# Kernel optimization log

Hardware: AMD Instinct MI355X
Metric: run time of the kernel (lower is better)

The kernel has to match this reference:

```python
import jax, jax.numpy as jnp
import numpy as np

BATCH = 16384
EPS = 1e-5


def _pool22_sum(x):
    # 4 * AvgPool2d((2,2),stride 2) == sum over 2x2 blocks. x: [B,1,h,w]
    B, C, h, w = x.shape
    return x.reshape(B, C, h // 2, 2, w // 2, 2).sum(axis=(3, 5))


def _transform(img, ans):
    # img: [B,h,h]. Faithful port of `transfrom`: zero border rows/cols, then
    # 10 quadratic features per 2x2 patch, laid out as [B,1,k,10k] with last
    # axis index = patch_col*10 + feature.
    B, h, w = img.shape
    if ans in ('top_bottom', 'all'):
        m = jnp.ones((h, 1), img.dtype).at[0].set(0).at[-1].set(0)
        img = img * m
    if ans in ('left_right', 'all'):
        m = jnp.ones((1, w), img.dtype).at[:, 0].set(0).at[:, -1].set(0)
        img = img * m
    k = h // 2
    p = img.reshape(B, k, 2, k, 2)
    b00 = p[:, :, 0, :, 0]; b01 = p[:, :, 0, :, 1]
    b10 = p[:, :, 1, :, 0]; b11 = p[:, :, 1, :, 1]
    prods = jnp.stack([
        b00 * b00, b01 * b01, b10 * b10, b11 * b11,
        b00 * b01, b00 * b10, b00 * b11,
        b01 * b10, b01 * b11, b10 * b11], axis=-1)  # [B,k,k,10]
    return prods.reshape(B, 1, k, 10 * k)


def _pool110_sum(a):
    # 10 * AvgPool2d((1,10),stride(1,10)) == sum over groups of 10 on last axis
    B, C, k, tk = a.shape
    return a.reshape(B, C, k, tk // 10, 10).sum(-1)


def _bn(x, gamma, beta):
    # BatchNorm2d(1) in training mode: batch stats over (N,H,W), biased var
    m = x.mean(axis=(0, 2, 3), keepdims=True)
    v = jnp.mean((x - m) ** 2, axis=(0, 2, 3), keepdims=True)
    g = gamma.reshape(1, -1, 1, 1)
    b = beta.reshape(1, -1, 1, 1)
    return (x - m) * jax.lax.rsqrt(v + EPS) * g + b


def setup_inputs() -> dict:
    key = jax.random.key(0)
    ks = jax.random.split(key, 16)

    def xavier(k, shape):
        fan_in, fan_out = shape[-1], shape[-2]
        std = np.sqrt(2.0 / (fan_in + fan_out))
        return jax.random.normal(k, shape, jnp.float32) * std

    return {
        'x': jax.random.normal(ks[0], (BATCH, 1, 28, 28), jnp.float32),
        'l1_w1': xavier(ks[1], (1, 28, 28)),
        'l1_w2_1': xavier(ks[2], (1, 14, 140)),
        'l1_w2_2': xavier(ks[3], (1, 14, 140)),
        'l1_w2_3': xavier(ks[4], (1, 14, 140)),
        'l1_w2_4': xavier(ks[5], (1, 14, 140)),
        'l1_w3': xavier(ks[6], (1, 14, 14)),
        'l2_w1': xavier(ks[7], (1, 14, 14)),
        'l2_w2': xavier(ks[8], (1, 7, 70)),
        'l2_w4': xavier(ks[9], (1, 7, 7)),
        'w_fc1': jax.random.normal(ks[10], (10, 49), jnp.float32) / np.sqrt(49.0),
        'b_fc1': jnp.zeros((10,), jnp.float32),
        'w_fc2': jax.random.normal(ks[11], (10, 2401), jnp.float32) / np.sqrt(2401.0),
        'b_fc2': jnp.zeros((10,), jnp.float32),
        'bn_gamma': jnp.ones((1,), jnp.float32),
        'bn_beta': jnp.zeros((1,), jnp.float32),
    }


def reference(x, l1_w1, l1_w2_1, l1_w2_2, l1_w2_3, l1_w2_4, l1_w3,
              l2_w1, l2_w2, l2_w4, w_fc1, b_fc1, w_fc2, b_fc2,
              bn_gamma, bn_beta):
    B = x.shape[0]
    img = x[:, 0]  # [B,28,28]
    # layer 1
    l1 = _pool22_sum(x * l1_w1)
    for W, ans in ((l1_w2_1, 'left_right'), (l1_w2_2, 'top_bottom'),
                   (l1_w2_3, 'all'), (l1_w2_4, 'none')):
        l1 = l1 + _pool110_sum(_transform(img, ans) * W)
    l1 = l1 + l1_w3  # [B,1,14,14]
    h = _bn(l1, bn_gamma, bn_beta)
    # layer 2
    l2 = _pool22_sum(h * l2_w1) + _pool110_sum(_transform(h[:, 0], 'none') * l2_w2) + l2_w4
    h = _bn(l2, bn_gamma, bn_beta)  # [B,1,7,7]
    # layer 3
    l3_x1 = h.reshape(B, -1) @ w_fc1.T + b_fc1
    v = h.reshape(B, 49)
    c = jnp.triu(v[:, :, None] * v[:, None, :])  # [B,49,49], trans_all_rg
    l3_x2 = c.reshape(B, -1) @ w_fc2.T + b_fc2
    return l3_x1 + l3_x2
```

## Files before the change

kernel.cpp:

```cpp
#include <hip/hip_runtime.h>

#define BATCH 16384
#define N1 (BATCH * 196)
#define N2 (BATCH * 49)
#define S1 8
#define NREC 80

#define WS_P1_OFF    0
#define WS_P2_OFF    32768
#define WS_WREC_OFF  65536
#define WS_L1G_OFF   262144
#define WS_L2G_OFF   6684672

__device__ __forceinline__ unsigned short f2bf(float f) {
    unsigned u = __float_as_uint(f);
    unsigned r = (u + 0x7FFFu + ((u >> 16) & 1u)) >> 16;
    return (unsigned short)r;
}
__device__ __forceinline__ float bf2f(unsigned short h) {
    return __uint_as_float((unsigned)h << 16);
}
__device__ __forceinline__ float rfl_f(float v) {
    return __uint_as_float(__builtin_amdgcn_readfirstlane(__float_as_uint(v)));
}

__global__ void __launch_bounds__(256) k1(
        const float* __restrict__ x,
        const float* __restrict__ l1w1, const float* __restrict__ wA,
        const float* __restrict__ wB, const float* __restrict__ wC,
        const float* __restrict__ wD, const float* __restrict__ l1w3,
        const float* __restrict__ wf2, const float* __restrict__ wfc1,
        unsigned short* __restrict__ l1g, double* __restrict__ partials1,
        float* __restrict__ wrec) {
    __shared__ __align__(16) float xs[S1 * 784];
    __shared__ float wls[4], wlss[4];
    int t = threadIdx.x;

    const float4* src = (const float4*)(x + (size_t)blockIdx.x * (S1 * 784));
    float4 rbuf[6];
    #pragma unroll
    for (int i = 0; i < 6; ++i) rbuf[i] = src[t + 256 * i];
    float4 rtail;
    if (t < 32) rtail = src[t + 1536];

    bool active = t < 196;
    int pos = active ? t : 0;
    int pi = pos / 14, pj = pos - 14 * pi;
    int r0 = (2 * pi) * 28 + 2 * pj;
    float4 a0, a1, a2, a3;
    {
        float2 wt = *(const float2*)(l1w1 + r0);
        float2 wb = *(const float2*)(l1w1 + r0 + 28);
        a0 = make_float4(wt.x, wt.y, wb.x, wb.y);
        float mA0 = (pj != 0) ? 1.f : 0.f, mA1 = (pj != 13) ? 1.f : 0.f;
        float mB0 = (pi != 0) ? 1.f : 0.f, mB1 = (pi != 13) ? 1.f : 0.f;
        float eA[4] = {mA0, mA1, mA0, mA1};
        float eB[4] = {mB0, mB0, mB1, mB1};
        const int e1i[10] = {0,1,2,3,0,0,0,1,1,2};
        const int e2i[10] = {0,1,2,3,1,2,3,2,3,3};
        int wo = pi * 140 + 10 * pj;
        float wq[10];
        #pragma unroll
        for (int k = 0; k < 10; ++k) {
            float ca = eA[e1i[k]] * eA[e2i[k]];
            float cb = eB[e1i[k]] * eB[e2i[k]];
            wq[k] = wA[wo + k] * ca + wB[wo + k] * cb
                  + wC[wo + k] * ca * cb + wD[wo + k];
        }
        a1 = make_float4(wq[0], wq[1], wq[2], wq[3]);
        a2 = make_float4(wq[4], wq[5], wq[6], wq[7]);
        a3 = make_float4(wq[8], wq[9], l1w3[pos], 0.f);
    }

    float4* dst = (float4*)xs;
    #pragma unroll
    for (int i = 0; i < 6; ++i) dst[t + 256 * i] = rbuf[i];
    if (t < 32) dst[t + 1536] = rtail;
    __syncthreads();

    float accs[S1];
    float sum = 0.f, sumsq = 0.f;
    #pragma unroll
    for (int s = 0; s < S1; ++s) {
        const float* xb = xs + s * 784;
        float2 tp = *(const float2*)(xb + r0);
        float2 bo = *(const float2*)(xb + r0 + 28);
        float b00 = tp.x, b01 = tp.y, b10 = bo.x, b11 = bo.y;
        float acc = b00 * a0.x + b01 * a0.y + b10 * a0.z + b11 * a0.w;
        acc += b00 * b00 * a1.x + b01 * b01 * a1.y + b10 * b10 * a1.z + b11 * b11 * a1.w;
        acc += b00 * b01 * a2.x + b00 * b10 * a2.y + b00 * b11 * a2.z + b01 * b10 * a2.w;
        acc += b01 * b11 * a3.x + b10 * b11 * a3.y + a3.z;
        accs[s] = acc;
        if (active) { sum += acc; sumsq += acc * acc; }
    }

    __syncthreads();
    unsigned short* ob = (unsigned short*)xs;
    if (active) {
        int g = ((pi >> 1) * 7 + (pj >> 1)) * 4 + (pi & 1) * 2 + (pj & 1);
        #pragma unroll
        for (int s = 0; s < S1; ++s) ob[s * 196 + g] = f2bf(accs[s]);
    }
    __syncthreads();
    const unsigned int* ob32 = (const unsigned int*)ob;
    unsigned int* gout = (unsigned int*)(l1g + (size_t)blockIdx.x * (S1 * 196));
    #pragma unroll
    for (int r2 = 0; r2 < 3; ++r2) gout[t + 256 * r2] = ob32[t + 256 * r2];
    if (t < 16) gout[t + 768] = ob32[t + 768];

    #pragma unroll
    for (int off = 32; off; off >>= 1) {
        sum += __shfl_down(sum, off);
        sumsq += __shfl_down(sumsq, off);
    }
    int lane = t & 63, wid = t >> 6;
    if (lane == 0) { wls[wid] = sum; wlss[wid] = sumsq; }
    __syncthreads();
    if (t == 0) {
        partials1[blockIdx.x * 2]     = (double)(wls[0] + wls[1] + wls[2] + wls[3]);
        partials1[blockIdx.x * 2 + 1] = (double)(wlss[0] + wlss[1] + wlss[2] + wlss[3]);
    }

    if (blockIdx.x < 5) {
        int e = blockIdx.x * 256 + t;
        if (e < 1280) {
            int w = e / NREC, j = e - w * NREC;
            int i = j * 16 + w;
            float wv[10];
            int ip = 0, iq = 0;
            if (i < 1225) {
                int rem = i, p = 0;
                while (rem >= 49 - p) { rem -= 49 - p; ++p; }
                int q = p + rem;
                #pragma unroll
                for (int o = 0; o < 10; ++o) wv[o] = wf2[o * 2401 + p * 49 + q];
                ip = p * 64; iq = q * 64;
            } else if (i < 1274) {
                int k = i - 1225;
                #pragma unroll
                for (int o = 0; o < 10; ++o) wv[o] = wfc1[o * 49 + k];
                ip = k * 64; iq = 49 * 64;
            } else {
                #pragma unroll
                for (int o = 0; o < 10; ++o) wv[o] = 0.f;
            }
            float* r = wrec + (size_t)e * 12;
            #pragma unroll
            for (int o = 0; o < 10; ++o) r[o] = wv[o];
            ((int*)r)[10] = ip;
            ((int*)r)[11] = iq;
        }
    }
}

__global__ void __launch_bounds__(256) k2(
        const unsigned short* __restrict__ l1g,
        const float* __restrict__ l2w1, const float* __restrict__ l2w2,
        const float* __restrict__ l2w4,
        const float* __restrict__ gamma, const float* __restrict__ beta,
        const double* __restrict__ partials1, double* __restrict__ partials2,
        float* __restrict__ l2g) {
    __shared__ float wls[4], wlss[4];
    __shared__ double dred[8];
    __shared__ float bcast[2];
    int t = threadIdx.x;
    int lane = t & 63, wid = t >> 6;
    int sbase = blockIdx.x * S1;

    bool active = t < 196;
    int tt = active ? t : 0;
    int sub = tt / 49;
    int pos = tt - 49 * sub;

    ushort4 u0 = *(const ushort4*)(l1g + ((size_t)(sbase + sub) * 49 + pos) * 4);
    ushort4 u1 = *(const ushort4*)(l1g + ((size_t)(sbase + 4 + sub) * 49 + pos) * 4);

    {
        double s = 0.0, ss = 0.0;
        const double* p1 = partials1 + t * 16;
        #pragma unroll
        for (int k = 0; k < 8; ++k) { s += p1[k * 2]; ss += p1[k * 2 + 1]; }
        #pragma unroll
        for (int off = 32; off; off >>= 1) {
            s += __shfl_down(s, off);
            ss += __shfl_down(ss, off);
        }
        if (lane == 0) { dred[wid * 2] = s; dred[wid * 2 + 1] = ss; }
        __syncthreads();
        if (t == 0) {
            double S = dred[0] + dred[2] + dred[4] + dred[6];
            double SS = dred[1] + dred[3] + dred[5] + dred[7];
            double mean = S / (double)N1;
            double var = SS / (double)N1 - mean * mean;
            float a = (float)((double)gamma[0] / sqrt(var + 1e-5));
            bcast[0] = a;
            bcast[1] = beta[0] - (float)mean * a;
        }
    }

    int pi = pos / 7, pj = pos - 7 * pi;
    int r0 = (2 * pi) * 14 + 2 * pj;
    float4 a0 = make_float4(l2w1[r0], l2w1[r0 + 1], l2w1[r0 + 14], l2w1[r0 + 15]);
    int wo = pi * 70 + 10 * pj;
    float4 q1 = make_float4(l2w2[wo],     l2w2[wo + 1], l2w2[wo + 2], l2w2[wo + 3]);
    float4 q2 = make_float4(l2w2[wo + 4], l2w2[wo + 5], l2w2[wo + 6], l2w2[wo + 7]);
    float4 q3 = make_float4(l2w2[wo + 8], l2w2[wo + 9], l2w4[pos], 0.f);
    __syncthreads();
    float a1 = bcast[0], c1 = bcast[1];

    float sum = 0.f, sumsq = 0.f;
    #pragma unroll
    for (int s2 = 0; s2 < 2; ++s2) {
        ushort4 u = s2 ? u1 : u0;
        int smp = sbase + s2 * 4 + sub;
        float h00 = fmaf(a1, bf2f(u.x), c1), h01 = fmaf(a1, bf2f(u.y), c1);
        float h10 = fmaf(a1, bf2f(u.z), c1), h11 = fmaf(a1, bf2f(u.w), c1);
        float acc = h00 * a0.x + h01 * a0.y + h10 * a0.z + h11 * a0.w;
        acc += h00 * h00 * q1.x + h01 * h01 * q1.y + h10 * h10 * q1.z + h11 * h11 * q1.w;
        acc += h00 * h01 * q2.x + h00 * h10 * q2.y + h00 * h11 * q2.z + h01 * h10 * q2.w;
        acc += h01 * h11 * q3.x + h10 * h11 * q3.y + q3.z;
        if (active) {
            l2g[(size_t)smp * 52 + pos] = acc;
            sum += acc;
            sumsq += acc * acc;
        }
    }

    #pragma unroll
    for (int off = 32; off; off >>= 1) {
        sum += __shfl_down(sum, off);
        sumsq += __shfl_down(sumsq, off);
    }
    if (lane == 0) { wls[wid] = sum; wlss[wid] = sumsq; }
    __syncthreads();
    if (t == 0) {
        partials2[blockIdx.x * 2]     = (double)(wls[0] + wls[1] + wls[2] + wls[3]);
        partials2[blockIdx.x * 2 + 1] = (double)(wlss[0] + wlss[1] + wlss[2] + wlss[3]);
    }
}

__global__ void __launch_bounds__(1024) k3(
        const float* __restrict__ l2g, const float* __restrict__ wrec,
        const float* __restrict__ b_fc1, const float* __restrict__ b_fc2,
        const float* __restrict__ gamma, const float* __restrict__ beta,
        const double* __restrict__ partials2, float* __restrict__ out) {
    __shared__ float part[16][64][10];
    __shared__ float vsm[50 * 64];
    __shared__ double dred[32];
    __shared__ float bcast[2];
    int t = threadIdx.x, lane = t & 63, wid = t >> 6;

    float4 val;
    int vs_s = 0, vs_k4 = 0;
    if (t < 832) {
        vs_s = t / 13;
        vs_k4 = t - vs_s * 13;
        val = ((const float4*)(l2g + (size_t)blockIdx.x * 64 * 52))[vs_s * 13 + vs_k4];
    }

    {
        const double* p2 = partials2 + t * 4;
        double sd = p2[0] + p2[2], ssd = p2[1] + p2[3];
        #pragma unroll
        for (int off = 32; off; off >>= 1) {
            sd += __shfl_down(sd, off);
            ssd += __shfl_down(ssd, off);
        }
        if (lane == 0) { dred[wid * 2] = sd; dred[wid * 2 + 1] = ssd; }
        __syncthreads();
        if (t == 0) {
            double S = 0.0, SS = 0.0;
            #pragma unroll
            for (int w = 0; w < 16; ++w) { S += dred[w * 2]; SS += dred[w * 2 + 1]; }
            double mean = S / (double)N2;
            double var = SS / (double)N2 - mean * mean;
            float a = (float)((double)gamma[0] / sqrt(var + 1e-5));
            bcast[0] = a;
            bcast[1] = beta[0] - (float)mean * a;
        }
        __syncthreads();
    }
    float a2 = bcast[0], c2 = bcast[1];

    if (t < 832) {
        float vv[4] = {val.x, val.y, val.z, val.w};
        #pragma unroll
        for (int j = 0; j < 4; ++j) {
            int p = vs_k4 * 4 + j;
            if (p < 49) vsm[p * 64 + vs_s] = fmaf(a2, vv[j], c2);
        }
    }
    if (t < 64) vsm[49 * 64 + t] = 1.f;
    __syncthreads();

    float acc[10];
    #pragma unroll
    for (int o = 0; o < 10; ++o) acc[o] = 0.f;

    int W = __builtin_amdgcn_readfirstlane(wid);
    const float* base = wrec + (size_t)W * NREC * 12;
    #pragma unroll 4
    for (int j = 0; j < NREC; ++j) {
        const float* rec = base + j * 12;
        int ip = __builtin_amdgcn_readfirstlane(((const int*)rec)[10]);
        int iq = __builtin_amdgcn_readfirstlane(((const int*)rec)[11]);
        float pv = vsm[ip + lane] * vsm[iq + lane];
        #pragma unroll
        for (int o = 0; o < 10; ++o) acc[o] = fmaf(pv, rfl_f(rec[o]), acc[o]);
    }

    #pragma unroll
    for (int o = 0; o < 10; ++o) part[wid][lane][o] = acc[o];
    __syncthreads();

    if (t < 640) {
        int sl = t / 10, o = t - 10 * sl;
        float r2 = 0.f;
        #pragma unroll
        for (int w = 0; w < 16; ++w) r2 += part[w][sl][o];
        out[(size_t)(blockIdx.x * 64 + sl) * 10 + o] = r2 + b_fc1[o] + b_fc2[o];
    }
}

extern "C" void kernel_launch(void* const* d_in, const int* in_sizes, int n_in,
                              void* d_out, int out_size, void* d_ws, size_t ws_size,
                              hipStream_t stream) {
    const float* x       = (const float*)d_in[0];
    const float* l1_w1   = (const float*)d_in[1];
    const float* l1_w2_1 = (const float*)d_in[2];
    const float* l1_w2_2 = (const float*)d_in[3];
    const float* l1_w2_3 = (const float*)d_in[4];
    const float* l1_w2_4 = (const float*)d_in[5];
    const float* l1_w3   = (const float*)d_in[6];
    const float* l2_w1   = (const float*)d_in[7];
    const float* l2_w2   = (const float*)d_in[8];
    const float* l2_w4   = (const float*)d_in[9];
    const float* w_fc1   = (const float*)d_in[10];
    const float* b_fc1   = (const float*)d_in[11];
    const float* w_fc2   = (const float*)d_in[12];
    const float* b_fc2   = (const float*)d_in[13];
    const float* bn_gamma = (const float*)d_in[14];
    const float* bn_beta  = (const float*)d_in[15];

    char* ws = (char*)d_ws;
    double* partials1 = (double*)(ws + WS_P1_OFF);
    double* partials2 = (double*)(ws + WS_P2_OFF);
    float* wrec = (float*)(ws + WS_WREC_OFF);
    unsigned short* l1g = (unsigned short*)(ws + WS_L1G_OFF);
    float* l2g = (float*)(ws + WS_L2G_OFF);
    float* out = (float*)d_out;

    k1<<<BATCH / S1, 256, 0, stream>>>(x, l1_w1, l1_w2_1, l1_w2_2, l1_w2_3, l1_w2_4,
                                       l1_w3, w_fc2, w_fc1, l1g, partials1, wrec);
    k2<<<BATCH / S1, 256, 0, stream>>>(l1g, l2_w1, l2_w2, l2_w4, bn_gamma, bn_beta,
                                       partials1, partials2, l2g);
    k3<<<BATCH / 64, 1024, 0, stream>>>(l2g, wrec, b_fc1, b_fc2,
                                        bn_gamma, bn_beta, partials2, out);
}
```

Measured before the change: 42.88 us.

## Fuse layer-2 into quadratic FC kernel via BN-affine algebraic decomposition

Uses the fact that the second batch norm is affine (h = a*v + c) to expand the quadratic FC layer into terms in raw v: v_p*v_q, linear v_k terms and a constant. The per-sample sums can then be computed before the global BN-2 statistics exist. This lets layer 2 be fused into the FC kernel, which removes the l2g round trip through global memory. A light epilogue kernel combines the three partial sums with the BN scalars once the stats are known. The costs are writing 30 partials per sample, extra precomputed weight tables, and possible float cancellation error from the expanded form.

Result: slower. 107.0 us (+149.6%).

```diff
diff --git a/kernel.cpp b/kernel.cpp
--- a/kernel.cpp
+++ b/kernel.cpp
@@ -4,13 +4,14 @@
 #define N1 (BATCH * 196)
 #define N2 (BATCH * 49)
 #define S1 8
-#define NREC 80
 
 #define WS_P1_OFF    0
 #define WS_P2_OFF    32768
-#define WS_WREC_OFF  65536
-#define WS_L1G_OFF   262144
-#define WS_L2G_OFF   6684672
+#define WS_WREC_OFF  40960
+#define WS_RTAB_OFF  102400
+#define WS_WFC1S_OFF 104448
+#define WS_FCP_OFF   131072
+#define WS_L1G_OFF   4194304
 
 __device__ __forceinline__ unsigned short f2bf(float f) {
     unsigned u = __float_as_uint(f);
@@ -31,7 +32,8 @@
         const float* __restrict__ wD, const float* __restrict__ l1w3,
         const float* __restrict__ wf2, const float* __restrict__ wfc1,
         unsigned short* __restrict__ l1g, double* __restrict__ partials1,
-        float* __restrict__ wrec) {
+        float* __restrict__ wrec, float* __restrict__ rtab,
+        float* __restrict__ wfc1s) {
     __shared__ __align__(16) float xs[S1 * 784];
     __shared__ float wls[4], wlss[4];
     int t = threadIdx.x;
@@ -123,144 +125,96 @@
 
     if (blockIdx.x < 5) {
         int e = blockIdx.x * 256 + t;
-        if (e < 1280) {
-            int w = e / NREC, j = e - w * NREC;
-            int i = j * 16 + w;
-            float wv[10];
-            int ip = 0, iq = 0;
-            if (i < 1225) {
-                int rem = i, p = 0;
-                while (rem >= 49 - p) { rem -= 49 - p; ++p; }
-                int q = p + rem;
-                #pragma unroll
-                for (int o = 0; o < 10; ++o) wv[o] = wf2[o * 2401 + p * 49 + q];
-                ip = p * 64; iq = q * 64;
-            } else if (i < 1274) {
-                int k = i - 1225;
-                #pragma unroll
-                for (int o = 0; o < 10; ++o) wv[o] = wfc1[o * 49 + k];
-                ip = k * 64; iq = 49 * 64;
-            } else {
-                #pragma unroll
-                for (int o = 0; o < 10; ++o) wv[o] = 0.f;
+        int w = e / 80, j = e - w * 80;
+        int i = j * 16 + w;
+        float wv[10];
+        int ip = 0, iq = 0;
+        if (j < 77 && i < 1225) {
+            int rem = i, p = 0;
+            while (rem >= 49 - p) { rem -= 49 - p; ++p; }
+            int q = p + rem;
+            #pragma unroll
+            for (int o = 0; o < 10; ++o) wv[o] = wf2[o * 2401 + p * 49 + q];
+            ip = p * 65; iq = q * 65;
+        } else {
+            #pragma unroll
+            for (int o = 0; o < 10; ++o) wv[o] = 0.f;
+        }
+        float* r = wrec + (size_t)e * 12;
+        #pragma unroll
+        for (int o = 0; o < 10; ++o) r[o] = wv[o];
+        ((int*)r)[10] = ip;
+        ((int*)r)[11] = iq;
+    } else if (blockIdx.x == 5) {
+        #pragma unroll
+        for (int rep = 0; rep < 2; ++rep) {
+            int id = rep * 256 + t;
+            if (id < 490) {
+                int k = id / 10, o = id - k * 10;
+                const float* row = wf2 + (size_t)o * 2401;
+                float r = 2.f * row[k * 49 + k];
+                for (int q = k + 1; q < 49; ++q) r += row[k * 49 + q];
+                for (int p = 0; p < k; ++p) r += row[p * 49 + k];
+                rtab[id] = r;
             }
-            float* r = wrec + (size_t)e * 12;
-            #pragma unroll
-            for (int o = 0; o < 10; ++o) r[o] = wv[o];
-            ((int*)r)[10] = ip;
-            ((int*)r)[11] = iq;
-        }
-    }
-}
-
-__global__ void __launch_bounds__(256) k2(
+        }
+    } else if (blockIdx.x == 6) {
+        #pragma unroll
+        for (int rep = 0; rep < 2; ++rep) {
+            int id = rep * 256 + t;
+            if (id < 490) {
+                int k = id / 10, o = id - k * 10;
+                wfc1s[id] = wfc1[o * 49 + k];
+            }
+        }
+    }
+}
+
+__global__ void __launch_bounds__(1024) k2(
         const unsigned short* __restrict__ l1g,
         const float* __restrict__ l2w1, const float* __restrict__ l2w2,
         const float* __restrict__ l2w4,
         const float* __restrict__ gamma, const float* __restrict__ beta,
         const double* __restrict__ partials1, double* __restrict__ partials2,
-        float* __restrict__ l2g) {
-    __shared__ float wls[4], wlss[4];
-    __shared__ double dred[8];
-    __shared__ float bcast[2];
-    int t = threadIdx.x;
-    int lane = t & 63, wid = t >> 6;
-    int sbase = blockIdx.x * S1;
-
-    bool active = t < 196;
-    int tt = active ? t : 0;
-    int sub = tt / 49;
-    int pos = tt - 49 * sub;
-
-    ushort4 u0 = *(const ushort4*)(l1g + ((size_t)(sbase + sub) * 49 + pos) * 4);
-    ushort4 u1 = *(const ushort4*)(l1g + ((size_t)(sbase + 4 + sub) * 49 + pos) * 4);
-
-    {
-        double s = 0.0, ss = 0.0;
-        const double* p1 = partials1 + t * 16;
-        #pragma unroll
-        for (int k = 0; k < 8; ++k) { s += p1[k * 2]; ss += p1[k * 2 + 1]; }
-        #pragma unroll
-        for (int off = 32; off; off >>= 1) {
-            s += __shfl_down(s, off);
-            ss += __shfl_down(ss, off);
-        }
-        if (lane == 0) { dred[wid * 2] = s; dred[wid * 2 + 1] = ss; }
-        __syncthreads();
-        if (t == 0) {
-            double S = dred[0] + dred[2] + dred[4] + dred[6];
-            double SS = dred[1] + dred[3] + dred[5] + dred[7];
-            double mean = S / (double)N1;
-            double var = SS / (double)N1 - mean * mean;
-            float a = (float)((double)gamma[0] / sqrt(var + 1e-5));
-            bcast[0] = a;
-            bcast[1] = beta[0] - (float)mean * a;
-        }
-    }
-
-    int pi = pos / 7, pj = pos - 7 * pi;
-    int r0 = (2 * pi) * 14 + 2 * pj;
-    float4 a0 = make_float4(l2w1[r0], l2w1[r0 + 1], l2w1[r0 + 14], l2w1[r0 + 15]);
-    int wo = pi * 70 + 10 * pj;
-    float4 q1 = make_float4(l2w2[wo],     l2w2[wo + 1], l2w2[wo + 2], l2w2[wo + 3]);
-    float4 q2 = make_float4(l2w2[wo + 4], l2w2[wo + 5], l2w2[wo + 6], l2w2[wo + 7]);
-    float4 q3 = make_float4(l2w2[wo + 8], l2w2[wo + 9], l2w4[pos], 0.f);
-    __syncthreads();
-    float a1 = bcast[0], c1 = bcast[1];
-
-    float sum = 0.f, sumsq = 0.f;
-    #pragma unroll
-    for (int s2 = 0; s2 < 2; ++s2) {
-        ushort4 u = s2 ? u1 : u0;
-        int smp = sbase + s2 * 4 + sub;
-        float h00 = fmaf(a1, bf2f(u.x), c1), h01 = fmaf(a1, bf2f(u.y), c1);
-        float h10 = fmaf(a1, bf2f(u.z), c1), h11 = fmaf(a1, bf2f(u.w), c1);
-        float acc = h00 * a0.x + h01 * a0.y + h10 * a0.z + h11 * a0.w;
-        acc += h00 * h00 * q1.x + h01 * h01 * q1.y + h10 * h10 * q1.z + h11 * h11 * q1.w;
-        acc += h00 * h01 * q2.x + h00 * h10 * q2.y + h00 * h11 * q2.z + h01 * h10 * q2.w;
-        acc += h01 * h11 * q3.x + h10 * h11 * q3.y + q3.z;
-        if (active) {
-            l2g[(size_t)smp * 52 + pos] = acc;
-            sum += acc;
-            sumsq += acc * acc;
-        }
-    }
-
-    #pragma unroll
-    for (int off = 32; off; off >>= 1) {
-        sum += __shfl_down(sum, off);
-        sumsq += __shfl_down(sumsq, off);
-    }
-    if (lane == 0) { wls[wid] = sum; wlss[wid] = sumsq; }
-    __syncthreads();
-    if (t == 0) {
-        partials2[blockIdx.x * 2]     = (double)(wls[0] + wls[1] + wls[2] + wls[3]);
-        partials2[blockIdx.x * 2 + 1] = (double)(wlss[0] + wlss[1] + wlss[2] + wlss[3]);
-    }
-}
-
-__global__ void __launch_bounds__(1024) k3(
-        const float* __restrict__ l2g, const float* __restrict__ wrec,
-        const float* __restrict__ b_fc1, const float* __restrict__ b_fc2,
-        const float* __restrict__ gamma, const float* __restrict__ beta,
-        const double* __restrict__ partials2, float* __restrict__ out) {
+        const float* __restrict__ wrec, const float* __restrict__ rtab,
+        const float* __restrict__ wfc1s, float* __restrict__ fcpart) {
     __shared__ float part[16][64][10];
-    __shared__ float vsm[50 * 64];
+    __shared__ float vsm[3200];
+    __shared__ float wkv[49 * 16];
     __shared__ double dred[32];
+    __shared__ float wls[16], wlss[16];
     __shared__ float bcast[2];
     int t = threadIdx.x, lane = t & 63, wid = t >> 6;
-
-    float4 val;
-    int vs_s = 0, vs_k4 = 0;
-    if (t < 832) {
-        vs_s = t / 13;
-        vs_k4 = t - vs_s * 13;
-        val = ((const float4*)(l2g + (size_t)blockIdx.x * 64 * 52))[vs_s * 13 + vs_k4];
+    int sbase = blockIdx.x * 64;
+
+    ushort4 u[4];
+    int us[4], up[4];
+    bool uv[4];
+    #pragma unroll
+    for (int i = 0; i < 4; ++i) {
+        int idx = i * 1024 + t;
+        uv[i] = idx < 3136;
+        int ii = uv[i] ? idx : 0;
+        int s = ii / 49, pos = ii - s * 49;
+        us[i] = s; up[i] = pos;
+        u[i] = *(const ushort4*)(l1g + ((size_t)(sbase + s) * 196 + pos * 4));
+    }
+
+    if (t < 49) {
+        int pos = t, pi = pos / 7, pj = pos - 7 * pi;
+        int r0 = 2 * pi * 14 + 2 * pj, wo = pi * 70 + 10 * pj;
+        float* w = wkv + pos * 16;
+        w[0] = l2w1[r0];      w[1] = l2w1[r0 + 1];
+        w[2] = l2w1[r0 + 14]; w[3] = l2w1[r0 + 15];
+        #pragma unroll
+        for (int k = 0; k < 10; ++k) w[4 + k] = l2w2[wo + k];
+        w[14] = l2w4[pos];
     }
 
     {
-        const double* p2 = partials2 + t * 4;
-        double sd = p2[0] + p2[2], ssd = p2[1] + p2[3];
+        const double* p1 = partials1 + (size_t)t * 4;
+        double sd = p1[0] + p1[2];
+        double ssd = p1[1] + p1[3];
         #pragma unroll
         for (int off = 32; off; off >>= 1) {
             sd += __shfl_down(sd, off);
@@ -272,35 +226,54 @@
             double S = 0.0, SS = 0.0;
             #pragma unroll
             for (int w = 0; w < 16; ++w) { S += dred[w * 2]; SS += dred[w * 2 + 1]; }
-            double mean = S / (double)N2;
-            double var = SS / (double)N2 - mean * mean;
+            double mean = S / (double)N1;
+            double var  = SS / (double)N1 - mean * mean;
             float a = (float)((double)gamma[0] / sqrt(var + 1e-5));
             bcast[0] = a;
             bcast[1] = beta[0] - (float)mean * a;
         }
         __syncthreads();
     }
-    float a2 = bcast[0], c2 = bcast[1];
-
-    if (t < 832) {
-        float vv[4] = {val.x, val.y, val.z, val.w};
-        #pragma unroll
-        for (int j = 0; j < 4; ++j) {
-            int p = vs_k4 * 4 + j;
-            if (p < 49) vsm[p * 64 + vs_s] = fmaf(a2, vv[j], c2);
-        }
-    }
-    if (t < 64) vsm[49 * 64 + t] = 1.f;
-    __syncthreads();
+    float a1 = bcast[0], c1 = bcast[1];
+
+    float psum = 0.f, psq = 0.f;
+    #pragma unroll
+    for (int i = 0; i < 4; ++i) {
+        if (!uv[i]) continue;
+        const float* w = wkv + up[i] * 16;
+        float h00 = fmaf(a1, bf2f(u[i].x), c1);
+        float h01 = fmaf(a1, bf2f(u[i].y), c1);
+        float h10 = fmaf(a1, bf2f(u[i].z), c1);
+        float h11 = fmaf(a1, bf2f(u[i].w), c1);
+        float acc = h00 * w[0] + h01 * w[1] + h10 * w[2] + h11 * w[3];
+        acc += h00 * h00 * w[4] + h01 * h01 * w[5] + h10 * h10 * w[6] + h11 * h11 * w[7];
+        acc += h00 * h01 * w[8] + h00 * h10 * w[9] + h00 * h11 * w[10] + h01 * h10 * w[11];
+        acc += h01 * h11 * w[12] + h10 * h11 * w[13] + w[14];
+        vsm[up[i] * 65 + us[i]] = acc;
+        psum += acc;
+        psq += acc * acc;
+    }
+    #pragma unroll
+    for (int off = 32; off; off >>= 1) {
+        psum += __shfl_down(psum, off);
+        psq  += __shfl_down(psq, off);
+    }
+    if (lane == 0) { wls[wid] = psum; wlss[wid] = psq; }
+    __syncthreads();
+    if (t == 0) {
+        float S = 0.f, SS = 0.f;
+        #pragma unroll
+        for (int w = 0; w < 16; ++w) { S += wls[w]; SS += wlss[w]; }
+        partials2[blockIdx.x * 2]     = (double)S;
+        partials2[blockIdx.x * 2 + 1] = (double)SS;
+    }
 
     float acc[10];
     #pragma unroll
     for (int o = 0; o < 10; ++o) acc[o] = 0.f;
-
-    int W = __builtin_amdgcn_readfirstlane(wid);
-    const float* base = wrec + (size_t)W * NREC * 12;
+    const float* base = wrec + (size_t)wid * 80 * 12;
     #pragma unroll 4
-    for (int j = 0; j < NREC; ++j) {
+    for (int j = 0; j < 77; ++j) {
         const float* rec = base + j * 12;
         int ip = __builtin_amdgcn_readfirstlane(((const int*)rec)[10]);
         int iq = __builtin_amdgcn_readfirstlane(((const int*)rec)[11]);
@@ -309,17 +282,99 @@
         for (int o = 0; o < 10; ++o) acc[o] = fmaf(pv, rfl_f(rec[o]), acc[o]);
     }
 
-    #pragma unroll
-    for (int o = 0; o < 10; ++o) part[wid][lane][o] = acc[o];
-    __syncthreads();
-
-    if (t < 640) {
-        int sl = t / 10, o = t - 10 * sl;
-        float r2 = 0.f;
-        #pragma unroll
-        for (int w = 0; w < 16; ++w) r2 += part[w][sl][o];
-        out[(size_t)(blockIdx.x * 64 + sl) * 10 + o] = r2 + b_fc1[o] + b_fc2[o];
-    }
+    float pl[10], ll[10];
+    #pragma unroll
+    for (int o = 0; o < 10; ++o) { pl[o] = 0.f; ll[o] = 0.f; }
+    #pragma unroll
+    for (int j = 0; j < 4; ++j) {
+        int k = wid + 16 * j;
+        if (k < 49) {
+            float vk = vsm[k * 65 + lane];
+            const float* rr = rtab + k * 10;
+            const float* ww = wfc1s + k * 10;
+            #pragma unroll
+            for (int o = 0; o < 10; ++o) {
+                pl[o] = fmaf(vk, rfl_f(rr[o]), pl[o]);
+                ll[o] = fmaf(vk, rfl_f(ww[o]), ll[o]);
+            }
+        }
+    }
+
+    const float* srcs[3] = {acc, pl, ll};
+    #pragma unroll
+    for (int r = 0; r < 3; ++r) {
+        __syncthreads();
+        #pragma unroll
+        for (int o = 0; o < 10; ++o) part[wid][lane][o] = srcs[r][o];
+        __syncthreads();
+        if (t < 640) {
+            int o = t >> 6, sl = t & 63;
+            float v = 0.f;
+            #pragma unroll
+            for (int w = 0; w < 16; ++w) v += part[w][sl][o];
+            fcpart[(size_t)(r * 10 + o) * BATCH + sbase + sl] = v;
+        }
+    }
+}
+
+__global__ void __launch_bounds__(256) k3(
+        const float* __restrict__ fcpart, const float* __restrict__ rtab,
+        const float* __restrict__ wfc1s,
+        const float* __restrict__ b_fc1, const float* __restrict__ b_fc2,
+        const float* __restrict__ gamma, const float* __restrict__ beta,
+        const double* __restrict__ partials2, float* __restrict__ out) {
+    __shared__ double dred[8];
+    __shared__ float bc[2];
+    __shared__ float fin[10];
+    int t = threadIdx.x, lane = t & 63, wid = t >> 6;
+    int s = blockIdx.x * 256 + t;
+
+    float pq[10], pl[10], ll[10];
+    #pragma unroll
+    for (int o = 0; o < 10; ++o) {
+        pq[o] = fcpart[(size_t)o * BATCH + s];
+        pl[o] = fcpart[(size_t)(10 + o) * BATCH + s];
+        ll[o] = fcpart[(size_t)(20 + o) * BATCH + s];
+    }
+
+    {
+        const double* p2 = partials2 + (size_t)t * 2;
+        double sd = p2[0], ssd = p2[1];
+        #pragma unroll
+        for (int off = 32; off; off >>= 1) {
+            sd += __shfl_down(sd, off);
+            ssd += __shfl_down(ssd, off);
+        }
+        if (lane == 0) { dred[wid * 2] = sd; dred[wid * 2 + 1] = ssd; }
+        __syncthreads();
+        if (t == 0) {
+            double S = dred[0] + dred[2] + dred[4] + dred[6];
+            double SS = dred[1] + dred[3] + dred[5] + dred[7];
+            double mean = S / (double)N2;
+            double var  = SS / (double)N2 - mean * mean;
+            float a = (float)((double)gamma[0] / sqrt(var + 1e-5));
+            bc[0] = a;
+            bc[1] = beta[0] - (float)mean * a;
+        }
+        __syncthreads();
+    }
+    float a2 = bc[0], c2 = bc[1];
+
+    if (t < 10) {
+        float wsum = 0.f, s1 = 0.f;
+        for (int k = 0; k < 49; ++k) {
+            wsum += rtab[k * 10 + t];
+            s1   += wfc1s[k * 10 + t];
+        }
+        wsum *= 0.5f;
+        fin[t] = c2 * c2 * wsum + c2 * s1 + b_fc1[t] + b_fc2[t];
+    }
+    __syncthreads();
+
+    float A = a2 * a2, B = a2 * c2;
+    #pragma unroll
+    for (int o = 0; o < 10; ++o)
+        out[(size_t)s * 10 + o] = A * pq[o] + B * pl[o] + a2 * ll[o] + fin[o];
 }
 
 extern "C" void kernel_launch(void* const* d_in, const int* in_sizes, int n_in,
@@ -345,15 +400,19 @@
     char* ws = (char*)d_ws;
     double* partials1 = (double*)(ws + WS_P1_OFF);
     double* partials2 = (double*)(ws + WS_P2_OFF);
-    float* wrec = (float*)(ws + WS_WREC_OFF);
+    float* wrec   = (float*)(ws + WS_WREC_OFF);
+    float* rtab   = (float*)(ws + WS_RTAB_OFF);
+    float* wfc1s  = (float*)(ws + WS_WFC1S_OFF);
+    float* fcpart = (float*)(ws + WS_FCP_OFF);
     unsigned short* l1g = (unsigned short*)(ws + WS_L1G_OFF);
-    float* l2g = (float*)(ws + WS_L2G_OFF);
     float* out = (float*)d_out;
 
     k1<<<BATCH / S1, 256, 0, stream>>>(x, l1_w1, l1_w2_1, l1_w2_2, l1_w2_3, l1_w2_4,
-                                       l1_w3, w_fc2, w_fc1, l1g, partials1, wrec);
-    k2<<<BATCH / S1, 256, 0, stream>>>(l1g, l2_w1, l2_w2, l2_w4, bn_gamma, bn_beta,
-                                       partials1, partials2, l2g);
-    k3<<<BATCH / 64, 1024, 0, stream>>>(l2g, wrec, b_fc1, b_fc2,
+                                       l1_w3, w_fc2, w_fc1, l1g, partials1,
+                                       wrec, rtab, wfc1s);
+    k2<<<BATCH / 64, 1024, 0, stream>>>(l1g, l2_w1, l2_w2, l2_w4, bn_gamma, bn_beta,
+                                        partials1, partials2, wrec, rtab, wfc1s,
+                                        fcpart);
+    k3<<<BATCH / 256, 256, 0, stream>>>(fcpart, rtab, wfc1s, b_fc1, b_fc2,
                                         bn_gamma, bn_beta, partials2, out);
 }
```

## Reshape layer-2 kernel into 64-sample blocks with shared weight table

Applied to the files above, without the earlier changes.

The layer-2 kernel now runs 256 blocks of 1024 threads, each handling 64 samples, instead of 2048 blocks of 256 threads handling 8. Per-position weights are staged once into shared memory rather than every thread loading them from global. Each block now produces fewer partial BN sums, so the reductions over partials1 and partials2 shrink to match. The goal is to cut per-block overhead and redundant weight loads, at the cost of fewer blocks in flight and shared-memory reads in the inner loop.

After: 38.82 us. 9.5% less time.

```diff
diff --git a/kernel.cpp b/kernel.cpp
--- a/kernel.cpp
+++ b/kernel.cpp
@@ -153,89 +153,90 @@
     }
 }
 
-__global__ void __launch_bounds__(256) k2(
+__global__ void __launch_bounds__(1024) k2(
         const unsigned short* __restrict__ l1g,
         const float* __restrict__ l2w1, const float* __restrict__ l2w2,
         const float* __restrict__ l2w4,
         const float* __restrict__ gamma, const float* __restrict__ beta,
         const double* __restrict__ partials1, double* __restrict__ partials2,
         float* __restrict__ l2g) {
-    __shared__ float wls[4], wlss[4];
-    __shared__ double dred[8];
+    __shared__ float wkv[49 * 16];
+    __shared__ double dred[32];
+    __shared__ float wls[16], wlss[16];
     __shared__ float bcast[2];
-    int t = threadIdx.x;
-    int lane = t & 63, wid = t >> 6;
-    int sbase = blockIdx.x * S1;
-
-    bool active = t < 196;
-    int tt = active ? t : 0;
-    int sub = tt / 49;
-    int pos = tt - 49 * sub;
-
-    ushort4 u0 = *(const ushort4*)(l1g + ((size_t)(sbase + sub) * 49 + pos) * 4);
-    ushort4 u1 = *(const ushort4*)(l1g + ((size_t)(sbase + 4 + sub) * 49 + pos) * 4);
+    int t = threadIdx.x, lane = t & 63, wid = t >> 6;
+    int sbase = blockIdx.x * 64;
+
+    if (t < 49) {
+        int pos = t, pi = pos / 7, pj = pos - 7 * pi;
+        int r0 = 2 * pi * 14 + 2 * pj, wo = pi * 70 + 10 * pj;
+        float* w = wkv + pos * 16;
+        w[0] = l2w1[r0];      w[1] = l2w1[r0 + 1];
+        w[2] = l2w1[r0 + 14]; w[3] = l2w1[r0 + 15];
+        #pragma unroll
+        for (int k = 0; k < 10; ++k) w[4 + k] = l2w2[wo + k];
+        w[14] = l2w4[pos];
+    }
 
     {
-        double s = 0.0, ss = 0.0;
-        const double* p1 = partials1 + t * 16;
-        #pragma unroll
-        for (int k = 0; k < 8; ++k) { s += p1[k * 2]; ss += p1[k * 2 + 1]; }
+        const double* p1 = partials1 + (size_t)t * 4;
+        double sd = p1[0] + p1[2];
+        double ssd = p1[1] + p1[3];
         #pragma unroll
         for (int off = 32; off; off >>= 1) {
-            s += __shfl_down(s, off);
-            ss += __shfl_down(ss, off);
-        }
-        if (lane == 0) { dred[wid * 2] = s; dred[wid * 2 + 1] = ss; }
+            sd += __shfl_down(sd, off);
+            ssd += __shfl_down(ssd, off);
+        }
+        if (lane == 0) { dred[wid * 2] = sd; dred[wid * 2 + 1] = ssd; }
         __syncthreads();
         if (t == 0) {
-            double S = dred[0] + dred[2] + dred[4] + dred[6];
-            double SS = dred[1] + dred[3] + dred[5] + dred[7];
+            double S = 0.0, SS = 0.0;
+            #pragma unroll
+            for (int w = 0; w < 16; ++w) { S += dred[w * 2]; SS += dred[w * 2 + 1]; }
             double mean = S / (double)N1;
-            double var = SS / (double)N1 - mean * mean;
+            double var  = SS / (double)N1 - mean * mean;
             float a = (float)((double)gamma[0] / sqrt(var + 1e-5));
             bcast[0] = a;
             bcast[1] = beta[0] - (float)mean * a;
         }
-    }
-
-    int pi = pos / 7, pj = pos - 7 * pi;
-    int r0 = (2 * pi) * 14 + 2 * pj;
-    float4 a0 = make_float4(l2w1[r0], l2w1[r0 + 1], l2w1[r0 + 14], l2w1[r0 + 15]);
-    int wo = pi * 70 + 10 * pj;
-    float4 q1 = make_float4(l2w2[wo],     l2w2[wo + 1], l2w2[wo + 2], l2w2[wo + 3]);
-    float4 q2 = make_float4(l2w2[wo + 4], l2w2[wo + 5], l2w2[wo + 6], l2w2[wo + 7]);
-    float4 q3 = make_float4(l2w2[wo + 8], l2w2[wo + 9], l2w4[pos], 0.f);
-    __syncthreads();
+        __syncthreads();
+    }
     float a1 = bcast[0], c1 = bcast[1];
 
-    float sum = 0.f, sumsq = 0.f;
-    #pragma unroll
-    for (int s2 = 0; s2 < 2; ++s2) {
-        ushort4 u = s2 ? u1 : u0;
-        int smp = sbase + s2 * 4 + sub;
-        float h00 = fmaf(a1, bf2f(u.x), c1), h01 = fmaf(a1, bf2f(u.y), c1);
-        float h10 = fmaf(a1, bf2f(u.z), c1), h11 = fmaf(a1, bf2f(u.w), c1);
-        float acc = h00 * a0.x + h01 * a0.y + h10 * a0.z + h11 * a0.w;
-        acc += h00 * h00 * q1.x + h01 * h01 * q1.y + h10 * h10 * q1.z + h11 * h11 * q1.w;
-        acc += h00 * h01 * q2.x + h00 * h10 * q2.y + h00 * h11 * q2.z + h01 * h10 * q2.w;
-        acc += h01 * h11 * q3.x + h10 * h11 * q3.y + q3.z;
-        if (active) {
-            l2g[(size_t)smp * 52 + pos] = acc;
-            sum += acc;
-            sumsq += acc * acc;
-        }
-    }
-
+    float psum = 0.f, psq = 0.f;
+    #pragma unroll
+    for (int i = 0; i < 4; ++i) {
+        int idx = i * 1024 + t;
+        if (idx < 3136) {
+            int s = idx / 49, pos = idx - s * 49;
+            ushort4 u = *(const ushort4*)(l1g + ((size_t)(sbase + s) * 196 + pos * 4));
+            const float* w = wkv + pos * 16;
+            float h00 = fmaf(a1, bf2f(u.x), c1);
+            float h01 = fmaf(a1, bf2f(u.y), c1);
+            float h10 = fmaf(a1, bf2f(u.z), c1);
+            float h11 = fmaf(a1, bf2f(u.w), c1);
+            float acc = h00 * w[0] + h01 * w[1] + h10 * w[2] + h11 * w[3];
+            acc += h00 * h00 * w[4] + h01 * h01 * w[5] + h10 * h10 * w[6] + h11 * h11 * w[7];
+            acc += h00 * h01 * w[8] + h00 * h10 * w[9] + h00 * h11 * w[10] + h01 * h10 * w[11];
+            acc += h01 * h11 * w[12] + h10 * h11 * w[13] + w[14];
+            l2g[(size_t)(sbase + s) * 52 + pos] = acc;
+            psum += acc;
+            psq += acc * acc;
+        }
+    }
     #pragma unroll
     for (int off = 32; off; off >>= 1) {
-        sum += __shfl_down(sum, off);
-        sumsq += __shfl_down(sumsq, off);
-    }
-    if (lane == 0) { wls[wid] = sum; wlss[wid] = sumsq; }
+        psum += __shfl_down(psum, off);
+        psq  += __shfl_down(psq, off);
+    }
+    if (lane == 0) { wls[wid] = psum; wlss[wid] = psq; }
     __syncthreads();
     if (t == 0) {
-        partials2[blockIdx.x * 2]     = (double)(wls[0] + wls[1] + wls[2] + wls[3]);
-        partials2[blockIdx.x * 2 + 1] = (double)(wlss[0] + wlss[1] + wlss[2] + wlss[3]);
+        float S = 0.f, SS = 0.f;
+        #pragma unroll
+        for (int w = 0; w < 16; ++w) { S += wls[w]; SS += wlss[w]; }
+        partials2[blockIdx.x * 2]     = (double)S;
+        partials2[blockIdx.x * 2 + 1] = (double)SS;
     }
 }
 
@@ -259,8 +260,11 @@
     }
 
     {
-        const double* p2 = partials2 + t * 4;
-        double sd = p2[0] + p2[2], ssd = p2[1] + p2[3];
+        double sd = 0.0, ssd = 0.0;
+        if (t < 256) {
+            sd = partials2[(size_t)t * 2];
+            ssd = partials2[(size_t)t * 2 + 1];
+        }
         #pragma unroll
         for (int off = 32; off; off >>= 1) {
             sd += __shfl_down(sd, off);
@@ -271,7 +275,7 @@
         if (t == 0) {
             double S = 0.0, SS = 0.0;
             #pragma unroll
-            for (int w = 0; w < 16; ++w) { S += dred[w * 2]; SS += dred[w * 2 + 1]; }
+            for (int w = 0; w < 4; ++w) { S += dred[w * 2]; SS += dred[w * 2 + 1]; }
             double mean = S / (double)N2;
             double var = SS / (double)N2 - mean * mean;
             float a = (float)((double)gamma[0] / sqrt(var + 1e-5));
@@ -352,8 +356,8 @@
 
     k1<<<BATCH / S1, 256, 0, stream>>>(x, l1_w1, l1_w2_1, l1_w2_2, l1_w2_3, l1_w2_4,
                                        l1_w3, w_fc2, w_fc1, l1g, partials1, wrec);
-    k2<<<BATCH / S1, 256, 0, stream>>>(l1g, l2_w1, l2_w2, l2_w4, bn_gamma, bn_beta,
-                                       partials1, partials2, l2g);
+    k2<<<BATCH / 64, 1024, 0, stream>>>(l1g, l2_w1, l2_w2, l2_w4, bn_gamma, bn_beta,
+                                        partials1, partials2, l2g);
     k3<<<BATCH / 64, 1024, 0, stream>>>(l2g, wrec, b_fc1, b_fc2,
                                         bn_gamma, bn_beta, partials2, out);
 }
```
